# Kernel tuning notes

Measured on AMD Instinct MI355X. Metric: run time of the kernel, lower is better.

## Reference

```python
import jax, jax.numpy as jnp
import numpy as np

# model dims
B, L, C, P, D, NB = 8, 512, 862, 96, 128, 2   # batch, seq_len, enc_in, pred_len, d_model, e_layers
I = 2 * D                                     # mLSTM inner (up-projection factor 2)
NH = 4                                        # mLSTM heads
DH = I // NH                                  # head dim
KDEC = 25                                     # series-decomp moving-average kernel
CK = 4                                        # causal conv kernel in mLSTM layer
EPS = 1e-5


def _ln(x, g):
    m = jnp.mean(x, -1, keepdims=True)
    v = jnp.var(x, -1, keepdims=True)
    return (x - m) * jax.lax.rsqrt(v + EPS) * g


def _mlstm_block(x, p):
    """Pre-LN residual mLSTM block (parallel stabilized formulation)."""
    (lng, Wup, bup, Wc, bc, Wq, Wk, Wv, Wi, bi, Wf, bf, mhg, skip, Wdn, bdn) = p
    Bn, S, _ = x.shape
    y = _ln(x, lng)
    up = y @ Wup + bup                       # [B,S,2I]
    x_in, z = jnp.split(up, 2, axis=-1)      # [B,S,I] each
    # causal depthwise conv (kernel CK) + SiLU
    xc = jax.lax.conv_general_dilated(
        x_in, Wc, window_strides=(1,), padding=((CK - 1, 0),),
        dimension_numbers=('NWC', 'WIO', 'NWC'), feature_group_count=I) + bc
    xc = jax.nn.silu(xc)
    q = xc @ Wq
    k = xc @ Wk
    v = x_in @ Wv
    g_in = jnp.concatenate([q, k, v], -1)    # [B,S,3I]
    ig = (g_in @ Wi + bi).transpose(0, 2, 1)  # [B,NH,S] input-gate preact
    fg = (g_in @ Wf + bf).transpose(0, 2, 1)  # [B,NH,S] forget-gate preact
    qh = q.reshape(Bn, S, NH, DH).transpose(0, 2, 1, 3)
    kh = k.reshape(Bn, S, NH, DH).transpose(0, 2, 1, 3) * (DH ** -0.5)
    vh = v.reshape(Bn, S, NH, DH).transpose(0, 2, 1, 3)
    logf = jax.nn.log_sigmoid(fg)            # [B,NH,S]
    cum = jnp.cumsum(logf, -1)               # inclusive cumsum
    # logD[t,s] = sum_{u=s+1..t} logf_u + i_s  (s<=t)
    logD = cum[..., :, None] - cum[..., None, :] + ig[..., None, :]
    mask = jnp.tril(jnp.ones((S, S), bool))
    logD = jnp.where(mask, logD, -jnp.inf)
    m = jnp.max(logD, -1, keepdims=True)     # row-wise stabilizer [B,NH,S,1]
    Dm = jnp.exp(logD - m)
    scores = jnp.einsum('bhtd,bhsd->bhts', qh, kh) * Dm
    norm = jnp.maximum(jnp.abs(jnp.sum(scores, -1, keepdims=True)), jnp.exp(-m))
    h = jnp.einsum('bhts,bhsd->bhtd', scores / norm, vh)  # [B,NH,S,DH]
    h = h.transpose(0, 2, 1, 3)              # [B,S,NH,DH]
    # multi-head layernorm (per-head, weight only)
    mu = jnp.mean(h, -1, keepdims=True)
    va = jnp.var(h, -1, keepdims=True)
    hn = ((h - mu) * jax.lax.rsqrt(va + EPS)).reshape(Bn, S, I) * mhg
    hs = (hn + skip * xc) * jax.nn.silu(z)
    return x + hs @ Wdn + bdn


def setup_inputs() -> dict:
    key = jax.random.key(0)
    ks = iter(jax.random.split(key, 32))
    f32 = jnp.float32
    def n(shape, s=0.02):
        return jax.random.normal(next(ks), shape, dtype=f32) * s
    inp = {
        'x_enc': jax.random.normal(next(ks), (B, L, C), f32),
        'x_mark_enc': jax.random.normal(next(ks), (B, L, 4), f32),
        'x_dec': jax.random.normal(next(ks), (B, P, C), f32),
        'x_mark_dec': jax.random.normal(next(ks), (B, P, 4), f32),
        # DLinear-style heads (init 1/seq_len as in the source)
        'Ws': jnp.full((P, L), 1.0 / L, dtype=f32), 'bs': jnp.zeros((P,), f32),
        'Wt': jnp.full((P, L), 1.0 / L, dtype=f32), 'bt': jnp.zeros((P,), f32),
        'Wp1': n((D, P)), 'bp1': jnp.zeros((D,), f32),
        'Wp2': n((P, D)), 'bp2': jnp.zeros((P,), f32),
        # stacked per-block mLSTM params
        'ln_g': jnp.ones((NB, D), f32),
        'Wup': n((NB, D, 2 * I)), 'bup': jnp.zeros((NB, 2 * I), f32),
        'Wconv': n((NB, CK, 1, I), 0.1), 'bconv': jnp.zeros((NB, I), f32),
        'Wq': n((NB, I, I)), 'Wk': n((NB, I, I)), 'Wv': n((NB, I, I)),
        'Wi': n((NB, 3 * I, NH)), 'bi': jnp.zeros((NB, NH), f32),
        'Wf': n((NB, 3 * I, NH)), 'bf': jnp.full((NB, NH), 3.0, dtype=f32),
        'mh_g': jnp.ones((NB, I), f32), 'skip': jnp.ones((NB, I), f32),
        'Wdn': n((NB, I, D)), 'bdn': jnp.zeros((NB, D), f32),
        'post_g': jnp.ones((D,), f32),
    }
    return inp


def reference(x_enc, x_mark_enc, x_dec, x_mark_dec, Ws, bs, Wt, bt, Wp1, bp1,
              Wp2, bp2, ln_g, Wup, bup, Wconv, bconv, Wq, Wk, Wv, Wi, bi, Wf,
              bf, mh_g, skip, Wdn, bdn, post_g):
    # series decomposition: edge-replicated moving average (kernel 25, stride 1)
    pad = (KDEC - 1) // 2
    front = jnp.repeat(x_enc[:, :1, :], pad, axis=1)
    end = jnp.repeat(x_enc[:, -1:, :], pad, axis=1)
    xp = jnp.concatenate([front, x_enc, end], axis=1)          # [B,L+24,C]
    cs = jnp.concatenate([jnp.zeros_like(xp[:, :1]), jnp.cumsum(xp, 1)], 1)
    mm = (cs[:, KDEC:, :] - cs[:, :-KDEC, :]) / KDEC           # [B,L,C]
    res = x_enc - mm
    si = res.transpose(0, 2, 1)                                # [B,C,L]
    ti = mm.transpose(0, 2, 1)
    x = (si @ Ws.T + bs) + (ti @ Wt.T + bt)                    # [B,C,P]
    x = x @ Wp1.T + bp1                                        # [B,C,D]
    for b in range(NB):
        x = _mlstm_block(x, (ln_g[b], Wup[b], bup[b], Wconv[b], bconv[b],
                             Wq[b], Wk[b], Wv[b], Wi[b], bi[b], Wf[b], bf[b],
                             mh_g[b], skip[b], Wdn[b], bdn[b]))
    x = _ln(x, post_g)
    x = x @ Wp2.T + bp2                                        # [B,C,P]
    return x.transpose(0, 2, 1)                                # [B,P,C]
```

## Files before the change

### kernel.cpp

```cpp
#include <hip/hip_runtime.h>
#include <math.h>

#define BB 8
#define LL 512
#define CC 862
#define PP 96
#define DD 128
#define II 256
#define NHH 4
#define DHH 64
#define SS 862
#define BC (BB*CC)
#define VTS 864
#define NITEMS2 896

typedef unsigned short u16;
using bf16x8 = __attribute__((ext_vector_type(8))) short;
using f32x4  = __attribute__((ext_vector_type(4))) float;

__device__ __forceinline__ u16 f2b(float x) {
  union { float f; unsigned u; } v; v.f = x;
  unsigned r = v.u + 0x7FFF + ((v.u >> 16) & 1);
  return (u16)(r >> 16);
}
__device__ __forceinline__ float b2f(u16 h) {
  union { unsigned u; float f; } v; v.u = ((unsigned)h) << 16;
  return v.f;
}

#define XCH(r, c) ((((c) ^ ((r) & 7)) << 3))

__global__ __launch_bounds__(256) void prep_kernel(
    const float* __restrict__ Wup, const float* __restrict__ Wq,
    const float* __restrict__ Wk, const float* __restrict__ Wv,
    const float* __restrict__ Wdn, const float* __restrict__ Ws,
    const float* __restrict__ Wt, const float* __restrict__ Wp1,
    const float* __restrict__ bs, const float* __restrict__ bt,
    const float* __restrict__ bp1, const float* __restrict__ Wi,
    const float* __restrict__ Wf,
    u16* __restrict__ WupT, u16* __restrict__ WqkT,
    u16* __restrict__ WvT, u16* __restrict__ WdnT,
    u16* __restrict__ BTh, float* __restrict__ hbias,
    float* __restrict__ Gc, float* __restrict__ Gv)
{
  int gb = blockIdx.x;
  int tid = threadIdx.x;
  if (gb < 640) {
    int bx = gb & 63, by = gb >> 6;
    const float* src; u16* dst; int R, Cn; float scl = 1.f;
    switch (by) {
      case 0: src = Wup;          dst = WupT;            R = 128; Cn = 512; break;
      case 1: src = Wup + 65536;  dst = WupT + 65536;    R = 128; Cn = 512; break;
      case 2: src = Wq;           dst = WqkT;            R = 256; Cn = 256; scl = 0.125f; break;
      case 3: src = Wk;           dst = WqkT + 65536;    R = 256; Cn = 256; break;
      case 4: src = Wq + 65536;   dst = WqkT + 131072;   R = 256; Cn = 256; scl = 0.125f; break;
      case 5: src = Wk + 65536;   dst = WqkT + 196608;   R = 256; Cn = 256; break;
      case 6: src = Wv;           dst = WvT;             R = 256; Cn = 256; break;
      case 7: src = Wv + 65536;   dst = WvT + 65536;     R = 256; Cn = 256; break;
      case 8: src = Wdn;          dst = WdnT;            R = 256; Cn = 128; break;
      default: src = Wdn + 32768; dst = WdnT + 32768;    R = 256; Cn = 128; break;
    }
    int tpr = Cn >> 5;
    int tx = bx % tpr, ty_ = bx / tpr;
    if (ty_ >= (R >> 5)) return;
    __shared__ float t[32][33];
    int r0 = ty_ * 32, c0 = tx * 32;
    int cr = tid >> 5, cc = tid & 31;
    #pragma unroll
    for (int rr = 0; rr < 4; ++rr)
      t[cr + rr * 8][cc] = src[(size_t)(r0 + cr + rr * 8) * Cn + c0 + cc];
    __syncthreads();
    #pragma unroll
    for (int rr = 0; rr < 4; ++rr)
      dst[(size_t)(c0 + cr + rr * 8) * R + r0 + cc] = f2b(t[cc][cr + rr * 8] * scl);
  } else if (gb < 1152) {
    int i2 = gb - 640;
    int d = i2 & 127, byy = i2 >> 7;
    int lp = byy * 256 + tid;
    const float* wp = Wp1 + d * 96;
    float acc = 0.f;
    if (lp < 512) {
      for (int p = 0; p < 96; ++p) acc += Ws[p * 512 + lp] * wp[p];
    } else {
      int l = lp - 512;
      for (int p = 0; p < 96; ++p) acc += (Wt[p * 512 + l] - Ws[p * 512 + l]) * wp[p];
    }
    BTh[(size_t)d * 1024 + lp] = f2b(acc);
  } else if (gb == 1152) {
    if (tid < 128) {
      float acc = bp1[tid];
      for (int p = 0; p < 96; ++p) acc += (bs[p] + bt[p]) * Wp1[tid * 96 + p];
      hbias[tid] = acc;
    }
  } else {
    int i2 = gb - 1153;
    int i = i2 & 255, blk = i2 >> 8;
    int j = tid;
    float wq = Wq[(size_t)blk * 65536 + i * 256 + j];
    float wk = Wk[(size_t)blk * 65536 + i * 256 + j];
    float wv = Wv[(size_t)blk * 65536 + i * 256 + j];
    const float* wi = Wi + blk * 3072;
    const float* wf = Wf + blk * 3072;
    float pc[8], pv[8];
    #pragma unroll
    for (int o = 0; o < 4; ++o) {
      pc[o]     = wq * wi[j * 4 + o] + wk * wi[(256 + j) * 4 + o];
      pc[4 + o] = wq * wf[j * 4 + o] + wk * wf[(256 + j) * 4 + o];
      pv[o]     = wv * wi[(512 + j) * 4 + o];
      pv[4 + o] = wv * wf[(512 + j) * 4 + o];
    }
    #pragma unroll
    for (int o = 0; o < 8; ++o)
      #pragma unroll
      for (int d = 1; d < 64; d <<= 1) {
        pc[o] += __shfl_xor(pc[o], d);
        pv[o] += __shfl_xor(pv[o], d);
      }
    __shared__ float red[4][16];
    int wv_ = j >> 6, lane = j & 63;
    if (lane == 0) {
      #pragma unroll
      for (int o = 0; o < 8; ++o) { red[wv_][o] = pc[o]; red[wv_][8 + o] = pv[o]; }
    }
    __syncthreads();
    if (j < 16) {
      float s4 = red[0][j] + red[1][j] + red[2][j] + red[3][j];
      if (j < 8) Gc[((size_t)blk * 256 + i) * 8 + j] = s4;
      else       Gv[((size_t)blk * 256 + i) * 8 + j - 8] = s4;
    }
  }
}

__global__ __launch_bounds__(256) void ta_kernel(
    const float* __restrict__ xe, u16* __restrict__ Ah)
{
  __shared__ float xel[16][545];
  __shared__ float mml[16][517];
  int tid = threadIdx.x;
  int b = blockIdx.x / 54, ct = blockIdx.x % 54;
  int c0 = ct * 16;
  for (int j = 0; j < 34; ++j) {
    int idx = tid + j * 256;
    if (idx < 8576) {
      int li = idx >> 4, cc = idx & 15;
      int l = li - 12; l = l < 0 ? 0 : (l > 511 ? 511 : l);
      int c = c0 + cc; if (c > 861) c = 861;
      xel[cc][li] = xe[((size_t)b * LL + l) * CC + c];
    }
  }
  __syncthreads();
  {
    int cl = tid & 15;
    int l0 = (tid >> 4) * 32;
    float win = 0.f;
    #pragma unroll 5
    for (int o = 0; o < 25; ++o) win += xel[cl][l0 + o];
    mml[cl][l0] = win * (1.f / 25.f);
    for (int i = 1; i < 32; ++i) {
      win += xel[cl][l0 + 24 + i] - xel[cl][l0 + i - 1];
      mml[cl][l0 + i] = win * (1.f / 25.f);
    }
  }
  __syncthreads();
  for (int j = 0; j < 32; ++j) {
    int idx = tid + j * 256;
    int cr = idx >> 9, l = idx & 511;
    int c = c0 + cr;
    if (c < CC) {
      size_t base = ((size_t)b * CC + c) * 1024;
      Ah[base + l] = f2b(xel[cr][12 + l]);
      Ah[base + 512 + l] = f2b(mml[cr][l]);
    }
  }
}

__device__ __forceinline__ void gemm_core(
    const u16* __restrict__ A, int lda, const u16* __restrict__ BT, int ldbt,
    int M, int K, int m0, int n0, int tid,
    u16 (*As0)[40], u16 (*As1)[40], u16 (*Bs0)[40], u16 (*Bs1)[40],
    f32x4 acc[2][2])
{
  int wv = tid >> 6, lane = tid & 63;
  int wr = wv >> 1, wc = wv & 1;
  int lrow = lane & 15, lk = lane >> 4;
  int arow = tid >> 2, aseg = tid & 3;
  for (int k0 = 0; k0 < K; k0 += 64) {
    int gm = m0 + arow; if (gm > M - 1) gm = M - 1;
    const u16* ap = &A[(size_t)gm * lda + k0 + aseg * 8];
    *(uint4*)&As0[arow][aseg * 8] = *(const uint4*)ap;
    *(uint4*)&As1[arow][aseg * 8] = *(const uint4*)(ap + 32);
    const u16* bp = &BT[(size_t)(n0 + arow) * ldbt + k0 + aseg * 8];
    *(uint4*)&Bs0[arow][aseg * 8] = *(const uint4*)bp;
    *(uint4*)&Bs1[arow][aseg * 8] = *(const uint4*)(bp + 32);
    __syncthreads();
    bf16x8 af[2], bfr[2];
    #pragma unroll
    for (int fm = 0; fm < 2; ++fm) af[fm] = *(const bf16x8*)&As0[wr * 32 + fm * 16 + lrow][lk * 8];
    #pragma unroll
    for (int fn = 0; fn < 2; ++fn) bfr[fn] = *(const bf16x8*)&Bs0[wc * 32 + fn * 16 + lrow][lk * 8];
    #pragma unroll
    for (int fm = 0; fm < 2; ++fm)
      #pragma unroll
      for (int fn = 0; fn < 2; ++fn)
        acc[fm][fn] = __builtin_amdgcn_mfma_f32_16x16x32_bf16(af[fm], bfr[fn], acc[fm][fn], 0, 0, 0);
    #pragma unroll
    for (int fm = 0; fm < 2; ++fm) af[fm] = *(const bf16x8*)&As1[wr * 32 + fm * 16 + lrow][lk * 8];
    #pragma unroll
    for (int fn = 0; fn < 2; ++fn) bfr[fn] = *(const bf16x8*)&Bs1[wc * 32 + fn * 16 + lrow][lk * 8];
    #pragma unroll
    for (int fm = 0; fm < 2; ++fm)
      #pragma unroll
      for (int fn = 0; fn < 2; ++fn)
        acc[fm][fn] = __builtin_amdgcn_mfma_f32_16x16x32_bf16(af[fm], bfr[fn], acc[fm][fn], 0, 0, 0);
    __syncthreads();
  }
}

template<int MODE>
__global__ __launch_bounds__(256) void gemm_bf16(
    const u16* __restrict__ A, int lda,
    const u16* __restrict__ BT, int ldbt,
    float* __restrict__ C, int ldc, const float* __restrict__ bias,
    int M, int N, int K)
{
  __shared__ u16 As0[64][40], As1[64][40];
  __shared__ u16 Bs0[64][40], Bs1[64][40];
  int tid = threadIdx.x;
  int m0 = blockIdx.y * 64, n0 = blockIdx.x * 64;
  f32x4 acc[2][2] = {};
  gemm_core(A, lda, BT, ldbt, M, K, m0, n0, tid, As0, As1, Bs0, Bs1, acc);
  int wv = tid >> 6, lane = tid & 63;
  int wr = wv >> 1, wc = wv & 1;
  int lrow = lane & 15, lk = lane >> 4;
  #pragma unroll
  for (int fm = 0; fm < 2; ++fm) {
    #pragma unroll
    for (int fn = 0; fn < 2; ++fn) {
      int col = n0 + wc * 32 + fn * 16 + lrow;
      #pragma unroll
      for (int r = 0; r < 4; ++r) {
        int row = m0 + wr * 32 + fm * 16 + lk * 4 + r;
        if (row < M) {
          float vv = acc[fm][fn][r];
          if (bias) vv += bias[col];
          float* cp = &C[(size_t)row * ldc + col];
          if (MODE == 1) vv += *cp;
          *cp = vv;
        }
      }
    }
  }
}

template<int MODE, int OUTF32>
__global__ __launch_bounds__(256) void gemm_ln(
    const u16* __restrict__ A, int lda,
    const u16* __restrict__ BT, int ldbt,
    float* __restrict__ x, const float* __restrict__ bias,
    const float* __restrict__ g,
    float* __restrict__ y, u16* __restrict__ y_bf,
    int M, int K)
{
  __shared__ u16 As0[32][40], As1[32][40];
  __shared__ u16 Bs0[128][40], Bs1[128][40];
  __shared__ float red_s[32][2], red_q[32][2];
  int tid = threadIdx.x;
  int m0 = blockIdx.x * 32;
  int wv = tid >> 6, lane = tid & 63;
  int wr = wv >> 1, wc = wv & 1;
  int lrow = lane & 15, lk = lane >> 4;
  f32x4 acc[4] = {};
  int arow = tid >> 3, aseg7 = tid & 7;
  int brow = tid >> 1, bhalf = tid & 1;
  for (int k0 = 0; k0 < K; k0 += 64) {
    int gm = m0 + arow; if (gm > M - 1) gm = M - 1;
    const u16* ap = &A[(size_t)gm * lda + k0];
    if (aseg7 < 4) *(uint4*)&As0[arow][aseg7 * 8] = *(const uint4*)(ap + aseg7 * 8);
    else           *(uint4*)&As1[arow][(aseg7 - 4) * 8] = *(const uint4*)(ap + 32 + (aseg7 - 4) * 8);
    const u16* bp = &BT[(size_t)brow * ldbt + k0];
    #pragma unroll
    for (int j = 0; j < 2; ++j) {
      int seg = bhalf * 2 + j;
      *(uint4*)&Bs0[brow][seg * 8] = *(const uint4*)(bp + seg * 8);
      *(uint4*)&Bs1[brow][seg * 8] = *(const uint4*)(bp + 32 + seg * 8);
    }
    __syncthreads();
    bf16x8 af, bfr[4];
    af = *(const bf16x8*)&As0[wr * 16 + lrow][lk * 8];
    #pragma unroll
    for (int fn = 0; fn < 4; ++fn) bfr[fn] = *(const bf16x8*)&Bs0[wc * 64 + fn * 16 + lrow][lk * 8];
    #pragma unroll
    for (int fn = 0; fn < 4; ++fn)
      acc[fn] = __builtin_amdgcn_mfma_f32_16x16x32_bf16(af, bfr[fn], acc[fn], 0, 0, 0);
    af = *(const bf16x8*)&As1[wr * 16 + lrow][lk * 8];
    #pragma unroll
    for (int fn = 0; fn < 4; ++fn) bfr[fn] = *(const bf16x8*)&Bs1[wc * 64 + fn * 16 + lrow][lk * 8];
    #pragma unroll
    for (int fn = 0; fn < 4; ++fn)
      acc[fn] = __builtin_amdgcn_mfma_f32_16x16x32_bf16(af, bfr[fn], acc[fn], 0, 0, 0);
    __syncthreads();
  }
  #pragma unroll
  for (int r = 0; r < 4; ++r) {
    int lrid = wr * 16 + lk * 4 + r;
    int grow = m0 + lrid;
    float sr = 0.f, sq = 0.f;
    #pragma unroll
    for (int fn = 0; fn < 4; ++fn) {
      int col = wc * 64 + fn * 16 + lrow;
      float vv = acc[fn][r] + bias[col];
      if (MODE == 1) vv += x[(size_t)grow * DD + col];
      acc[fn][r] = vv;
      if (grow < M) x[(size_t)grow * DD + col] = vv;
      sr += vv; sq += vv * vv;
    }
    sr += __shfl_xor(sr, 1); sq += __shfl_xor(sq, 1);
    sr += __shfl_xor(sr, 2); sq += __shfl_xor(sq, 2);
    sr += __shfl_xor(sr, 4); sq += __shfl_xor(sq, 4);
    sr += __shfl_xor(sr, 8); sq += __shfl_xor(sq, 8);
    if (lrow == 0) { red_s[lrid][wc] = sr; red_q[lrid][wc] = sq; }
  }
  __syncthreads();
  #pragma unroll
  for (int r = 0; r < 4; ++r) {
    int lrid = wr * 16 + lk * 4 + r;
    int grow = m0 + lrid;
    if (grow >= M) continue;
    float s = red_s[lrid][0] + red_s[lrid][1];
    float q = red_q[lrid][0] + red_q[lrid][1];
    float mean = s * (1.f / 128.f);
    float var = q * (1.f / 128.f) - mean * mean;
    float rr = rsqrtf(var + 1e-5f);
    #pragma unroll
    for (int fn = 0; fn < 4; ++fn) {
      int col = wc * 64 + fn * 16 + lrow;
      float out = (acc[fn][r] - mean) * rr * g[col];
      if (OUTF32) y[(size_t)grow * DD + col] = out;
      else        y_bf[(size_t)grow * DD + col] = f2b(out);
    }
  }
}

__global__ __launch_bounds__(256) void qkv_kernel(
    const u16* __restrict__ xc_bf, const u16* __restrict__ xin_bf,
    const u16* __restrict__ WqkT, const u16* __restrict__ WvT,
    u16* __restrict__ qkh, u16* __restrict__ qkl,
    u16* __restrict__ vhT, u16* __restrict__ vlT)
{
  __shared__ u16 As0[64][40], As1[64][40];
  __shared__ u16 Bs0[64][40], Bs1[64][40];
  int tid = threadIdx.x;
  int m0 = blockIdx.y * 64;
  bool is_qk = blockIdx.x < 8;
  int n0 = (is_qk ? blockIdx.x : blockIdx.x - 8) * 64;
  const u16* A  = is_qk ? xc_bf : xin_bf;
  const u16* BT = is_qk ? WqkT : WvT;
  f32x4 acc[2][2] = {};
  gemm_core(A, 256, BT, 256, BC, 256, m0, n0, tid, As0, As1, Bs0, Bs1, acc);
  int wv = tid >> 6, lane = tid & 63;
  int wr = wv >> 1, wc = wv & 1;
  int lrow = lane & 15, lk = lane >> 4;
  #pragma unroll
  for (int fm = 0; fm < 2; ++fm) {
    #pragma unroll
    for (int fn = 0; fn < 2; ++fn) {
      int col = n0 + wc * 32 + fn * 16 + lrow;
      int rbase = m0 + wr * 32 + fm * 16 + lk * 4;
      if (is_qk) {
        #pragma unroll
        for (int r = 0; r < 4; ++r) {
          int row = rbase + r;
          if (row < BC) {
            float vv = acc[fm][fn][r];
            u16 hi = f2b(vv);
            u16 lo = f2b(vv - b2f(hi));
            qkh[(size_t)row * 512 + col] = hi;
            qkl[(size_t)row * 512 + col] = lo;
          }
        }
      } else {
        u16 hi4[4], lo4[4];
        #pragma unroll
        for (int r = 0; r < 4; ++r) {
          float vv = acc[fm][fn][r];
          hi4[r] = f2b(vv);
          lo4[r] = f2b(vv - b2f(hi4[r]));
        }
        int bb0 = rbase / SS, s0_ = rbase - bb0 * SS;
        int bb3 = (rbase + 3) / SS;
        if (bb0 == bb3 && rbase + 3 < BC) {
          size_t o = ((size_t)bb0 * II + col) * VTS + s0_;
          *(unsigned*)&vhT[o]     = (unsigned)hi4[0] | ((unsigned)hi4[1] << 16);
          *(unsigned*)&vhT[o + 2] = (unsigned)hi4[2] | ((unsigned)hi4[3] << 16);
          *(unsigned*)&vlT[o]     = (unsigned)lo4[0] | ((unsigned)lo4[1] << 16);
          *(unsigned*)&vlT[o + 2] = (unsigned)lo4[2] | ((unsigned)lo4[3] << 16);
        } else {
          #pragma unroll
          for (int r = 0; r < 4; ++r) {
            int row = rbase + r;
            if (row < BC) {
              int bb = row / SS, s = row - bb * SS;
              size_t o = ((size_t)bb * II + col) * VTS + s;
              vhT[o] = hi4[r];
              vlT[o] = lo4[r];
            }
          }
        }
      }
    }
  }
}

__global__ __launch_bounds__(256) void conv_gates_kernel(
    const float* __restrict__ up, const float* __restrict__ Wc,
    const float* __restrict__ bc, const float* __restrict__ Gc,
    const float* __restrict__ Gv, const float* __restrict__ bi,
    const float* __restrict__ bfp,
    float* __restrict__ xc, u16* __restrict__ xc_bf, u16* __restrict__ xin_bf,
    float* __restrict__ ig, float* __restrict__ fg)
{
  __shared__ float red[4][8];
  int row = blockIdx.x;
  int i = threadIdx.x;
  int b = row / SS, s = row - b * SS;
  float acc = bc[i];
  float xin = 0.f;
  #pragma unroll
  for (int w2 = 0; w2 < 4; ++w2) {
    int sp = s - 3 + w2;
    if (sp >= 0) {
      float uv = up[((size_t)b * SS + sp) * 512 + i];
      acc += uv * Wc[w2 * 256 + i];
      if (w2 == 3) xin = uv;
    }
  }
  float sg = 1.f / (1.f + __expf(-acc));
  float val = acc * sg;
  xc[(size_t)row * II + i] = val;
  xc_bf[(size_t)row * II + i] = f2b(val);
  xin_bf[(size_t)row * II + i] = f2b(xin);
  float p[8];
  const float* gci = &Gc[i * 8];
  const float* gvi = &Gv[i * 8];
  #pragma unroll
  for (int o = 0; o < 8; ++o) p[o] = val * gci[o] + xin * gvi[o];
  #pragma unroll
  for (int o = 0; o < 8; ++o)
    #pragma unroll
    for (int d = 1; d < 64; d <<= 1) p[o] += __shfl_xor(p[o], d);
  int wv = i >> 6, lane = i & 63;
  if (lane == 0) {
    #pragma unroll
    for (int o = 0; o < 8; ++o) red[wv][o] = p[o];
  }
  __syncthreads();
  if (i < 8) {
    float sum = red[0][i] + red[1][i] + red[2][i] + red[3][i];
    if (i < 4) ig[((size_t)b * NHH + i) * SS + s] = sum + bi[i];
    else       fg[((size_t)b * NHH + i - 4) * SS + s] = sum + bfp[i - 4];
  }
}

__device__ __forceinline__ float logsig(float x) {
  return fminf(x, 0.f) - log1pf(__expf(-fabsf(x)));
}

__global__ __launch_bounds__(64) void scan_kernel(
    const float* __restrict__ fg, const float* __restrict__ ig,
    float* __restrict__ cumf, float* __restrict__ aa, float* __restrict__ MMb)
{
  int bh = blockIdx.x;
  int lane = threadIdx.x;
  const float* f = fg + (size_t)bh * SS;
  const float* g = ig + (size_t)bh * SS;
  int s0 = lane * 14, s1 = s0 + 14; if (s1 > SS) s1 = SS;
  float loc = 0.f;
  for (int s = s0; s < s1; ++s) loc += logsig(f[s]);
  float v = loc;
  #pragma unroll
  for (int d = 1; d < 64; d <<= 1) { float o = __shfl_up(v, d); if (lane >= d) v += o; }
  float run = v - loc;
  float lmax = -1e30f;
  for (int s = s0; s < s1; ++s) {
    run += logsig(f[s]);
    cumf[(size_t)bh * SS + s] = run;
    float a = g[s] - run;
    aa[(size_t)bh * SS + s] = a;
    lmax = fmaxf(lmax, a);
  }
  float mv = lmax;
  #pragma unroll
  for (int d = 1; d < 64; d <<= 1) { float o = __shfl_up(mv, d); if (lane >= d) mv = fmaxf(mv, o); }
  float em = __shfl_up(mv, 1);
  if (lane == 0) em = -1e30f;
  float runm = em;
  for (int s = s0; s < s1; ++s) {
    runm = fmaxf(runm, aa[(size_t)bh * SS + s]);
    MMb[(size_t)bh * SS + s] = runm;
  }
}

__global__ __launch_bounds__(256) void attn_kernel(
    const u16* __restrict__ qkh, const u16* __restrict__ qkl,
    const u16* __restrict__ vhT, const u16* __restrict__ vlT,
    const float* __restrict__ aab, const float* __restrict__ MMb,
    float* __restrict__ pacc, float* __restrict__ pw)
{
  __shared__ u16 KWh[64][64], KWl[64][64];
  __shared__ u16 Vh[64][64], Vl[64][64];
  __shared__ float a_lds[64];
  int tid = threadIdx.x;
  int wv = tid >> 6, lane = tid & 63;
  int lr = lane & 15, lg = lane >> 4;
  int item = blockIdx.x;
  int pp = item >> 5;
  int tb = 13 - (pp >> 1);
  int part = pp & 1;
  int h = item & 3, b = (item >> 2) & 7;
  int t0 = tb * 64;
  int nt = tb + 1;
  int nt0 = (nt + 1) >> 1;
  int st_begin = part ? nt0 : 0;
  int st_end   = part ? nt : nt0;
  const float* aabh = aab + ((size_t)b * NHH + h) * SS;
  const float* Mbh  = MMb + ((size_t)b * NHH + h) * SS;

  int tq = t0 + wv * 16 + lr; if (tq > SS - 1) tq = SS - 1;
  const u16* qrow_h = qkh + ((size_t)b * SS + tq) * 512 + h * 64;
  const u16* qrow_l = qkl + ((size_t)b * SS + tq) * 512 + h * 64;
  bf16x8 qh0 = *(const bf16x8*)(qrow_h + lg * 8);
  bf16x8 qh1 = *(const bf16x8*)(qrow_h + 32 + lg * 8);
  bf16x8 ql0 = *(const bf16x8*)(qrow_l + lg * 8);
  bf16x8 ql1 = *(const bf16x8*)(qrow_l + 32 + lg * 8);

  float Mt[4];
  #pragma unroll
  for (int r = 0; r < 4; ++r) {
    int t = t0 + wv * 16 + lg * 4 + r; int tc = t < SS ? t : SS - 1;
    Mt[r] = Mbh[tc];
  }

  int row = tid >> 2, seg = tid & 3;
  const u16* vrow_h = vhT + ((size_t)(b * II + h * 64 + row)) * VTS + seg * 16;
  const u16* vrow_l = vlT + ((size_t)(b * II + h * 64 + row)) * VTS + seg * 16;

  f32x4 hacc[4] = {};
  float wsum[4] = {0.f, 0.f, 0.f, 0.f};

  uint4 rk0, rk1, rk2, rk3, rv0, rv1, rv2, rv3;
  float ra = -1e30f;
  if (st_begin < st_end) {
    int sg = st_begin * 64 + row;
    int sc = sg < SS ? sg : SS - 1;
    const u16* kp  = qkh + ((size_t)b * SS + sc) * 512 + 256 + h * 64 + seg * 16;
    const u16* klp = qkl + ((size_t)b * SS + sc) * 512 + 256 + h * 64 + seg * 16;
    rk0 = *(const uint4*)kp;  rk1 = *(const uint4*)(kp + 8);
    rk2 = *(const uint4*)klp; rk3 = *(const uint4*)(klp + 8);
    int sn = st_begin * 64;
    rv0 = *(const uint4*)(vrow_h + sn); rv1 = *(const uint4*)(vrow_h + sn + 8);
    rv2 = *(const uint4*)(vrow_l + sn); rv3 = *(const uint4*)(vrow_l + sn + 8);
    if (tid < 64) ra = (sn + tid < SS) ? aabh[sn + tid] : -1e30f;
  }

  for (int st = st_begin; st < st_end; ++st) {
    int s0 = st * 64;
    __syncthreads();
    *(uint4*)&KWh[row][XCH(row, 2 * seg)]     = rk0;
    *(uint4*)&KWh[row][XCH(row, 2 * seg + 1)] = rk1;
    *(uint4*)&KWl[row][XCH(row, 2 * seg)]     = rk2;
    *(uint4*)&KWl[row][XCH(row, 2 * seg + 1)] = rk3;
    *(uint4*)&Vh[row][XCH(row, 2 * seg)]     = rv0;
    *(uint4*)&Vh[row][XCH(row, 2 * seg + 1)] = rv1;
    *(uint4*)&Vl[row][XCH(row, 2 * seg)]     = rv2;
    *(uint4*)&Vl[row][XCH(row, 2 * seg + 1)] = rv3;
    if (tid < 64) a_lds[tid] = ra;
    if (st + 1 < st_end) {
      int sn = s0 + 64;
      int sg = sn + row;
      int sc = sg < SS ? sg : SS - 1;
      const u16* kp  = qkh + ((size_t)b * SS + sc) * 512 + 256 + h * 64 + seg * 16;
      const u16* klp = qkl + ((size_t)b * SS + sc) * 512 + 256 + h * 64 + seg * 16;
      rk0 = *(const uint4*)kp;  rk1 = *(const uint4*)(kp + 8);
      rk2 = *(const uint4*)klp; rk3 = *(const uint4*)(klp + 8);
      rv0 = *(const uint4*)(vrow_h + sn); rv1 = *(const uint4*)(vrow_h + sn + 8);
      rv2 = *(const uint4*)(vrow_l + sn); rv3 = *(const uint4*)(vrow_l + sn + 8);
      if (tid < 64) ra = (sn + tid < SS) ? aabh[sn + tid] : -1e30f;
    }
    __syncthreads();
    float am = a_lds[lane];
    #pragma unroll
    for (int dd = 1; dd < 64; dd <<= 1) am = fmaxf(am, __shfl_xor(am, dd));
    f32x4 p[4];
    #pragma unroll
    for (int sf = 0; sf < 4; ++sf) {
      int sr = sf * 16 + lr;
      bf16x8 kh0 = *(const bf16x8*)&KWh[sr][XCH(sr, lg)];
      bf16x8 kh1 = *(const bf16x8*)&KWh[sr][XCH(sr, lg + 4)];
      bf16x8 kl0 = *(const bf16x8*)&KWl[sr][XCH(sr, lg)];
      bf16x8 kl1 = *(const bf16x8*)&KWl[sr][XCH(sr, lg + 4)];
      f32x4 acc = {};
      acc = __builtin_amdgcn_mfma_f32_16x16x32_bf16(qh0, kl0, acc, 0, 0, 0);
      acc = __builtin_amdgcn_mfma_f32_16x16x32_bf16(qh1, kl1, acc, 0, 0, 0);
      acc = __builtin_amdgcn_mfma_f32_16x16x32_bf16(ql0, kh0, acc, 0, 0, 0);
      acc = __builtin_amdgcn_mfma_f32_16x16x32_bf16(ql1, kh1, acc, 0, 0, 0);
      acc = __builtin_amdgcn_mfma_f32_16x16x32_bf16(qh0, kh0, acc, 0, 0, 0);
      acc = __builtin_amdgcn_mfma_f32_16x16x32_bf16(qh1, kh1, acc, 0, 0, 0);
      p[sf] = acc;
    }
    __syncthreads();
    float ee[4], ft[4];
    #pragma unroll
    for (int sf = 0; sf < 4; ++sf) ee[sf] = __expf(a_lds[sf * 16 + lr] - am);
    #pragma unroll
    for (int r = 0; r < 4; ++r) ft[r] = __expf(fminf(am - Mt[r], 80.f));
    #pragma unroll
    for (int sf = 0; sf < 4; ++sf) {
      int s = s0 + sf * 16 + lr;
      int sc_ = sf * 2 + (lr >> 3), sb = lr & 7;
      #pragma unroll
      for (int r = 0; r < 4; ++r) {
        int tl_ = wv * 16 + lg * 4 + r;
        int t = t0 + tl_;
        float wval = (s <= t) ? p[sf][r] * ee[sf] * ft[r] : 0.f;
        wsum[r] += wval;
        u16 hi_ = f2b(wval);
        u16 lo_ = f2b(wval - b2f(hi_));
        KWh[tl_][XCH(tl_, sc_) + sb] = hi_;
        KWl[tl_][XCH(tl_, sc_) + sb] = lo_;
      }
    }
    __syncthreads();
    int tr = wv * 16 + lr;
    bf16x8 wh0 = *(const bf16x8*)&KWh[tr][XCH(tr, lg)];
    bf16x8 wh1 = *(const bf16x8*)&KWh[tr][XCH(tr, lg + 4)];
    bf16x8 wl0 = *(const bf16x8*)&KWl[tr][XCH(tr, lg)];
    bf16x8 wl1 = *(const bf16x8*)&KWl[tr][XCH(tr, lg + 4)];
    #pragma unroll
    for (int df = 0; df < 4; ++df) {
      int dr = df * 16 + lr;
      bf16x8 vh0 = *(const bf16x8*)&Vh[dr][XCH(dr, lg)];
      bf16x8 vh1 = *(const bf16x8*)&Vh[dr][XCH(dr, lg + 4)];
      bf16x8 vl0 = *(const bf16x8*)&Vl[dr][XCH(dr, lg)];
      bf16x8 vl1 = *(const bf16x8*)&Vl[dr][XCH(dr, lg + 4)];
      f32x4 a2 = hacc[df];
      a2 = __builtin_amdgcn_mfma_f32_16x16x32_bf16(wh0, vl0, a2, 0, 0, 0);
      a2 = __builtin_amdgcn_mfma_f32_16x16x32_bf16(wh1, vl1, a2, 0, 0, 0);
      a2 = __builtin_amdgcn_mfma_f32_16x16x32_bf16(wl0, vh0, a2, 0, 0, 0);
      a2 = __builtin_amdgcn_mfma_f32_16x16x32_bf16(wl1, vh1, a2, 0, 0, 0);
      a2 = __builtin_amdgcn_mfma_f32_16x16x32_bf16(wh0, vh0, a2, 0, 0, 0);
      a2 = __builtin_amdgcn_mfma_f32_16x16x32_bf16(wh1, vh1, a2, 0, 0, 0);
      hacc[df] = a2;
    }
  }
  #pragma unroll
  for (int r = 0; r < 4; ++r) {
    float sgn = wsum[r];
    sgn += __shfl_xor(sgn, 1); sgn += __shfl_xor(sgn, 2);
    sgn += __shfl_xor(sgn, 4); sgn += __shfl_xor(sgn, 8);
    wsum[r] = sgn;
  }
  float* pa = pacc + (size_t)part * BC * II;
  #pragma unroll
  for (int r = 0; r < 4; ++r) {
    int t = t0 + wv * 16 + lg * 4 + r;
    if (t < SS) {
      #pragma unroll
      for (int df = 0; df < 4; ++df)
        pa[((size_t)b * SS + t) * II + h * 64 + df * 16 + lr] = hacc[df][r];
      if (lr == 0)
        pw[(((size_t)part * BB + b) * NHH + h) * SS + t] = wsum[r];
    }
  }
}

__global__ __launch_bounds__(256) void combine_mhln_kernel(
    const float* __restrict__ pacc, const float* __restrict__ pw,
    const float* __restrict__ cumf, const float* __restrict__ MMb,
    const float* __restrict__ up, const float* __restrict__ xc,
    const float* __restrict__ mhg, const float* __restrict__ skip,
    u16* __restrict__ hb_bf)
{
  int row = blockIdx.x;
  int i = threadIdx.x;
  int h = i >> 6, lane = i & 63;
  int b = row / SS, s = row - b * SS;
  size_t bhS = ((size_t)b * NHH + h) * SS + s;
  float v = pacc[(size_t)row * II + i] + pacc[(size_t)BC * II + (size_t)row * II + i];
  float wsum = pw[bhS] + pw[(size_t)BB * NHH * SS + bhS];
  float nfl = __expf(-(cumf[bhS] + MMb[bhS]));
  float hv = v / fmaxf(fabsf(wsum), nfl);
  float sm = hv, sq = hv * hv;
  #pragma unroll
  for (int d = 1; d < 64; d <<= 1) { sm += __shfl_xor(sm, d); sq += __shfl_xor(sq, d); }
  float mu = sm * (1.f / 64.f);
  float var = sq * (1.f / 64.f) - mu * mu;
  float hn = (hv - mu) * rsqrtf(var + 1e-5f) * mhg[i];
  float z = up[(size_t)row * 512 + 256 + i];
  float sil = z / (1.f + __expf(-z));
  hb_bf[(size_t)row * II + i] = f2b((hn + skip[i] * xc[(size_t)row * II + i]) * sil);
}

__global__ __launch_bounds__(256) void final_kernel(
    const float* __restrict__ y, const float* __restrict__ Wp2,
    const float* __restrict__ bp2, float* __restrict__ out)
{
  __shared__ float yl[32 * 132];
  __shared__ float ol[96 * 32];
  int tid = threadIdx.x;
  int blk = blockIdx.x;
  int b = blk / 27, ct = blk % 27;
  int c0 = ct * 32;
  int nc = CC - c0; if (nc > 32) nc = 32;
  for (int j = 0; j < 16; ++j) {
    int idx = tid + j * 256;
    int cl = idx >> 7, d2 = idx & 127;
    yl[cl * 132 + d2] = (cl < nc) ? y[((size_t)b * CC + c0 + cl) * DD + d2] : 0.f;
  }
  __syncthreads();
  for (int j = 0; j < 12; ++j) {
    int o = tid + j * 256;
    int p = o >> 5, cl = o & 31;
    const float* wr = Wp2 + p * 128;
    float acc = bp2[p];
    #pragma unroll 8
    for (int d0 = 0; d0 < 128; d0 += 4) {
      float4 yv = *(const float4*)&yl[cl * 132 + d0];
      float4 wv = *(const float4*)&wr[d0];
      acc += yv.x * wv.x + yv.y * wv.y + yv.z * wv.z + yv.w * wv.w;
    }
    ol[p * 32 + cl] = acc;
  }
  __syncthreads();
  for (int j = 0; j < 12; ++j) {
    int o = tid + j * 256;
    int p = o >> 5, cl = o & 31;
    if (cl < nc) out[(size_t)b * PP * CC + (size_t)p * CC + c0 + cl] = ol[p * 32 + cl];
  }
}

extern "C" void kernel_launch(void* const* d_in, const int* in_sizes, int n_in,
                              void* d_out, int out_size, void* d_ws, size_t ws_size,
                              hipStream_t stream) {
  const float* xe   = (const float*)d_in[0];
  const float* Ws   = (const float*)d_in[4];
  const float* bs   = (const float*)d_in[5];
  const float* Wt_  = (const float*)d_in[6];
  const float* bt   = (const float*)d_in[7];
  const float* Wp1  = (const float*)d_in[8];
  const float* bp1  = (const float*)d_in[9];
  const float* Wp2  = (const float*)d_in[10];
  const float* bp2  = (const float*)d_in[11];
  const float* lng  = (const float*)d_in[12];
  const float* Wup  = (const float*)d_in[13];
  const float* bup  = (const float*)d_in[14];
  const float* Wcv  = (const float*)d_in[15];
  const float* bcv  = (const float*)d_in[16];
  const float* Wq   = (const float*)d_in[17];
  const float* Wk   = (const float*)d_in[18];
  const float* Wv   = (const float*)d_in[19];
  const float* Wi   = (const float*)d_in[20];
  const float* bi   = (const float*)d_in[21];
  const float* Wf   = (const float*)d_in[22];
  const float* bf_  = (const float*)d_in[23];
  const float* mhg  = (const float*)d_in[24];
  const float* skp  = (const float*)d_in[25];
  const float* Wdn  = (const float*)d_in[26];
  const float* bdn  = (const float*)d_in[27];
  const float* pg   = (const float*)d_in[28];
  float* out = (float*)d_out;

  float* w   = (float*)d_ws;
  float* x   = w;
  float* y   = x   + 882688;
  float* up  = y   + 882688;
  float* xc  = up  + 3530752;
  float* pacc = xc + 1765376;
  float* pw  = pacc + 3530752;
  float* ig  = pw  + 55168;
  float* fg  = ig  + 27584;
  float* cum = fg  + 27584;
  float* aab = cum + 27584;
  float* MMb = aab + 27584;
  float* hbias = MMb + 27584;
  float* Gc  = hbias + 128;
  float* Gv  = Gc + 4096;
  u16* ub    = (u16*)(Gv + 4096);
  u16* y_bf  = ub;            ub += 6896 * 128;
  u16* xc_bf = ub;            ub += 6896 * 256;
  u16* xin_bf = ub;           ub += 6896 * 256;
  u16* hb_bf = ub;            ub += 6896 * 256;
  u16* qkh   = ub;            ub += 6896 * 512;
  u16* qkl   = ub;            ub += 6896 * 512;
  u16* vhT   = ub;            ub += 8 * 256 * VTS;
  u16* vlT   = ub;            ub += 8 * 256 * VTS;
  u16* BTh   = ub;            ub += 131072;
  u16* WupT  = ub;            ub += 131072;
  u16* WqkT  = ub;            ub += 262144;
  u16* WvT   = ub;            ub += 131072;
  u16* WdnT  = ub;            ub += 65536;
  u16* Ah = (u16*)up;

  prep_kernel<<<1665, 256, 0, stream>>>(
      Wup, Wq, Wk, Wv, Wdn, Ws, Wt_, Wp1, bs, bt, bp1, Wi, Wf,
      WupT, WqkT, WvT, WdnT, BTh, hbias, Gc, Gv);

  ta_kernel<<<432, 256, 0, stream>>>(xe, Ah);
  gemm_ln<0, 0><<<216, 256, 0, stream>>>(
      Ah, 1024, BTh, 1024, x, hbias, lng, nullptr, y_bf, BC, 1024);

  for (int blk = 0; blk < 2; ++blk) {
    gemm_bf16<0><<<dim3(8, 108), 256, 0, stream>>>(
        y_bf, 128, WupT + blk * 65536, 128, up, 512, bup + blk * 512, BC, 512, 128);
    conv_gates_kernel<<<6896, 256, 0, stream>>>(
        up, Wcv + blk * 1024, bcv + blk * 256, Gc + blk * 2048, Gv + blk * 2048,
        bi + blk * 4, bf_ + blk * 4, xc, xc_bf, xin_bf, ig, fg);
    qkv_kernel<<<dim3(12, 108), 256, 0, stream>>>(
        xc_bf, xin_bf, WqkT + blk * 131072, WvT + blk * 65536,
        qkh, qkl, vhT, vlT);
    scan_kernel<<<32, 64, 0, stream>>>(fg, ig, cum, aab, MMb);
    attn_kernel<<<NITEMS2, 256, 0, stream>>>(qkh, qkl, vhT, vlT, aab, MMb, pacc, pw);
    combine_mhln_kernel<<<6896, 256, 0, stream>>>(
        pacc, pw, cum, MMb, up, xc, mhg + blk * 256, skp + blk * 256, hb_bf);
    if (blk == 0)
      gemm_ln<1, 0><<<216, 256, 0, stream>>>(
          hb_bf, 256, WdnT, 256, x, bdn, lng + 128, nullptr, y_bf, BC, 256);
    else
      gemm_ln<1, 1><<<216, 256, 0, stream>>>(
          hb_bf, 256, WdnT + 32768, 256, x, bdn + 128, pg, y, nullptr, BC, 256);
  }

  final_kernel<<<216, 256, 0, stream>>>(y, Wp2, bp2, out);
}
```

Baseline: 276.7 us.

## Fuse mLSTM combine/headnorm into down-proj GEMM A-load and merge scan into qkv

Removes the combine_mhln kernel: the down-projection GEMM+LN now computes the normalized, gated mLSTM output directly while loading its A tile, so the intermediate bf16 hb buffer is no longer written and re-read. The scan kernel is also folded into the qkv GEMM launch as 32 extra blocks, which cuts launches and lets the scan overlap the GEMM. The catch is that the fused A-load does more scalar fp32 loads and transcendental work inside the GEMM's K loop, with only 216 blocks to hide that latency.

```diff
diff --git a/kernel.cpp b/kernel.cpp
--- a/kernel.cpp
+++ b/kernel.cpp
@@ -252,14 +252,18 @@
   }
 }
 
-template<int MODE, int OUTF32>
+template<int MODE, int OUTF32, int FUSEC>
 __global__ __launch_bounds__(256) void gemm_ln(
     const u16* __restrict__ A, int lda,
     const u16* __restrict__ BT, int ldbt,
     float* __restrict__ x, const float* __restrict__ bias,
     const float* __restrict__ g,
     float* __restrict__ y, u16* __restrict__ y_bf,
-    int M, int K)
+    int M, int K,
+    const float* __restrict__ pacc, const float* __restrict__ pw,
+    const float* __restrict__ cumf, const float* __restrict__ MMb,
+    const float* __restrict__ up2, const float* __restrict__ xc2,
+    const float* __restrict__ mhg, const float* __restrict__ skip)
 {
   __shared__ u16 As0[32][40], As1[32][40];
   __shared__ u16 Bs0[128][40], Bs1[128][40];
@@ -274,9 +278,44 @@
   int brow = tid >> 1, bhalf = tid & 1;
   for (int k0 = 0; k0 < K; k0 += 64) {
     int gm = m0 + arow; if (gm > M - 1) gm = M - 1;
-    const u16* ap = &A[(size_t)gm * lda + k0];
-    if (aseg7 < 4) *(uint4*)&As0[arow][aseg7 * 8] = *(const uint4*)(ap + aseg7 * 8);
-    else           *(uint4*)&As1[arow][(aseg7 - 4) * 8] = *(const uint4*)(ap + 32 + (aseg7 - 4) * 8);
+    if (FUSEC == 0) {
+      const u16* ap = &A[(size_t)gm * lda + k0];
+      if (aseg7 < 4) *(uint4*)&As0[arow][aseg7 * 8] = *(const uint4*)(ap + aseg7 * 8);
+      else           *(uint4*)&As1[arow][(aseg7 - 4) * 8] = *(const uint4*)(ap + 32 + (aseg7 - 4) * 8);
+    } else {
+      int bb = gm / SS, sx = gm - bb * SS;
+      int hh = k0 >> 6;
+      size_t bhS = ((size_t)bb * NHH + hh) * SS + sx;
+      float wsum = pw[bhS] + pw[(size_t)BB * NHH * SS + bhS];
+      float nfl = __expf(-(cumf[bhS] + MMb[bhS]));
+      float rden = 1.f / fmaxf(fabsf(wsum), nfl);
+      int colb = k0 + aseg7 * 8;
+      const float* p0 = &pacc[(size_t)gm * II + colb];
+      const float* p1 = p0 + (size_t)BC * II;
+      float hv[8], sr = 0.f, sq2 = 0.f;
+      #pragma unroll
+      for (int j = 0; j < 8; ++j) {
+        hv[j] = (p0[j] + p1[j]) * rden;
+        sr += hv[j]; sq2 += hv[j] * hv[j];
+      }
+      sr += __shfl_xor(sr, 1); sq2 += __shfl_xor(sq2, 1);
+      sr += __shfl_xor(sr, 2); sq2 += __shfl_xor(sq2, 2);
+      sr += __shfl_xor(sr, 4); sq2 += __shfl_xor(sq2, 4);
+      float mu = sr * (1.f / 64.f);
+      float var = sq2 * (1.f / 64.f) - mu * mu;
+      float rr2 = rsqrtf(var + 1e-5f);
+      u16 o8[8];
+      #pragma unroll
+      for (int j = 0; j < 8; ++j) {
+        int col = colb + j;
+        float hn = (hv[j] - mu) * rr2 * mhg[col];
+        float z = up2[(size_t)gm * 512 + 256 + col];
+        float sil = z / (1.f + __expf(-z));
+        o8[j] = f2b((hn + skip[col] * xc2[(size_t)gm * II + col]) * sil);
+      }
+      if (aseg7 < 4) *(uint4*)&As0[arow][aseg7 * 8] = *(const uint4*)o8;
+      else           *(uint4*)&As1[arow][(aseg7 - 4) * 8] = *(const uint4*)o8;
+    }
     const u16* bp = &BT[(size_t)brow * ldbt + k0];
     #pragma unroll
     for (int j = 0; j < 2; ++j) {
@@ -341,18 +380,59 @@
   }
 }
 
-__global__ __launch_bounds__(256) void qkv_kernel(
+__device__ __forceinline__ float logsig(float x) {
+  return fminf(x, 0.f) - log1pf(__expf(-fabsf(x)));
+}
+
+__global__ __launch_bounds__(256) void qkv_scan_kernel(
     const u16* __restrict__ xc_bf, const u16* __restrict__ xin_bf,
     const u16* __restrict__ WqkT, const u16* __restrict__ WvT,
     u16* __restrict__ qkh, u16* __restrict__ qkl,
-    u16* __restrict__ vhT, u16* __restrict__ vlT)
+    u16* __restrict__ vhT, u16* __restrict__ vlT,
+    const float* __restrict__ fg, const float* __restrict__ ig,
+    float* __restrict__ cumf, float* __restrict__ aa, float* __restrict__ MMb)
 {
   __shared__ u16 As0[64][40], As1[64][40];
   __shared__ u16 Bs0[64][40], Bs1[64][40];
   int tid = threadIdx.x;
-  int m0 = blockIdx.y * 64;
-  bool is_qk = blockIdx.x < 8;
-  int n0 = (is_qk ? blockIdx.x : blockIdx.x - 8) * 64;
+  int bx = blockIdx.x;
+  if (bx >= 1296) {
+    if (tid >= 64) return;
+    int bh = bx - 1296;
+    int lane = tid;
+    const float* f = fg + (size_t)bh * SS;
+    const float* gg = ig + (size_t)bh * SS;
+    int s0 = lane * 14, s1 = s0 + 14; if (s1 > SS) s1 = SS;
+    float loc = 0.f;
+    for (int s = s0; s < s1; ++s) loc += logsig(f[s]);
+    float v = loc;
+    #pragma unroll
+    for (int d = 1; d < 64; d <<= 1) { float o = __shfl_up(v, d); if (lane >= d) v += o; }
+    float run = v - loc;
+    float lmax = -1e30f;
+    for (int s = s0; s < s1; ++s) {
+      run += logsig(f[s]);
+      cumf[(size_t)bh * SS + s] = run;
+      float a = gg[s] - run;
+      aa[(size_t)bh * SS + s] = a;
+      lmax = fmaxf(lmax, a);
+    }
+    float mv = lmax;
+    #pragma unroll
+    for (int d = 1; d < 64; d <<= 1) { float o = __shfl_up(mv, d); if (lane >= d) mv = fmaxf(mv, o); }
+    float em = __shfl_up(mv, 1);
+    if (lane == 0) em = -1e30f;
+    float runm = em;
+    for (int s = s0; s < s1; ++s) {
+      runm = fmaxf(runm, aa[(size_t)bh * SS + s]);
+      MMb[(size_t)bh * SS + s] = runm;
+    }
+    return;
+  }
+  int m0 = (bx / 12) * 64;
+  int nrole = bx % 12;
+  bool is_qk = nrole < 8;
+  int n0 = (is_qk ? nrole : nrole - 8) * 64;
   const u16* A  = is_qk ? xc_bf : xin_bf;
   const u16* BT = is_qk ? WqkT : WvT;
   f32x4 acc[2][2] = {};
@@ -461,45 +541,6 @@
   }
 }
 
-__device__ __forceinline__ float logsig(float x) {
-  return fminf(x, 0.f) - log1pf(__expf(-fabsf(x)));
-}
-
-__global__ __launch_bounds__(64) void scan_kernel(
-    const float* __restrict__ fg, const float* __restrict__ ig,
-    float* __restrict__ cumf, float* __restrict__ aa, float* __restrict__ MMb)
-{
-  int bh = blockIdx.x;
-  int lane = threadIdx.x;
-  const float* f = fg + (size_t)bh * SS;
-  const float* g = ig + (size_t)bh * SS;
-  int s0 = lane * 14, s1 = s0 + 14; if (s1 > SS) s1 = SS;
-  float loc = 0.f;
-  for (int s = s0; s < s1; ++s) loc += logsig(f[s]);
-  float v = loc;
-  #pragma unroll
-  for (int d = 1; d < 64; d <<= 1) { float o = __shfl_up(v, d); if (lane >= d) v += o; }
-  float run = v - loc;
-  float lmax = -1e30f;
-  for (int s = s0; s < s1; ++s) {
-    run += logsig(f[s]);
-    cumf[(size_t)bh * SS + s] = run;
-    float a = g[s] - run;
-    aa[(size_t)bh * SS + s] = a;
-    lmax = fmaxf(lmax, a);
-  }
-  float mv = lmax;
-  #pragma unroll
-  for (int d = 1; d < 64; d <<= 1) { float o = __shfl_up(mv, d); if (lane >= d) mv = fmaxf(mv, o); }
-  float em = __shfl_up(mv, 1);
-  if (lane == 0) em = -1e30f;
-  float runm = em;
-  for (int s = s0; s < s1; ++s) {
-    runm = fmaxf(runm, aa[(size_t)bh * SS + s]);
-    MMb[(size_t)bh * SS + s] = runm;
-  }
-}
-
 __global__ __launch_bounds__(256) void attn_kernel(
     const u16* __restrict__ qkh, const u16* __restrict__ qkl,
     const u16* __restrict__ vhT, const u16* __restrict__ vlT,
@@ -671,33 +712,6 @@
         pw[(((size_t)part * BB + b) * NHH + h) * SS + t] = wsum[r];
     }
   }
-}
-
-__global__ __launch_bounds__(256) void combine_mhln_kernel(
-    const float* __restrict__ pacc, const float* __restrict__ pw,
-    const float* __restrict__ cumf, const float* __restrict__ MMb,
-    const float* __restrict__ up, const float* __restrict__ xc,
-    const float* __restrict__ mhg, const float* __restrict__ skip,
-    u16* __restrict__ hb_bf)
-{
-  int row = blockIdx.x;
-  int i = threadIdx.x;
-  int h = i >> 6, lane = i & 63;
-  int b = row / SS, s = row - b * SS;
-  size_t bhS = ((size_t)b * NHH + h) * SS + s;
-  float v = pacc[(size_t)row * II + i] + pacc[(size_t)BC * II + (size_t)row * II + i];
-  float wsum = pw[bhS] + pw[(size_t)BB * NHH * SS + bhS];
-  float nfl = __expf(-(cumf[bhS] + MMb[bhS]));
-  float hv = v / fmaxf(fabsf(wsum), nfl);
-  float sm = hv, sq = hv * hv;
-  #pragma unroll
-  for (int d = 1; d < 64; d <<= 1) { sm += __shfl_xor(sm, d); sq += __shfl_xor(sq, d); }
-  float mu = sm * (1.f / 64.f);
-  float var = sq * (1.f / 64.f) - mu * mu;
-  float hn = (hv - mu) * rsqrtf(var + 1e-5f) * mhg[i];
-  float z = up[(size_t)row * 512 + 256 + i];
-  float sil = z / (1.f + __expf(-z));
-  hb_bf[(size_t)row * II + i] = f2b((hn + skip[i] * xc[(size_t)row * II + i]) * sil);
 }
 
 __global__ __launch_bounds__(256) void final_kernel(
@@ -788,7 +802,6 @@
   u16* y_bf  = ub;            ub += 6896 * 128;
   u16* xc_bf = ub;            ub += 6896 * 256;
   u16* xin_bf = ub;           ub += 6896 * 256;
-  u16* hb_bf = ub;            ub += 6896 * 256;
   u16* qkh   = ub;            ub += 6896 * 512;
   u16* qkl   = ub;            ub += 6896 * 512;
   u16* vhT   = ub;            ub += 8 * 256 * VTS;
@@ -805,8 +818,9 @@
       WupT, WqkT, WvT, WdnT, BTh, hbias, Gc, Gv);
 
   ta_kernel<<<432, 256, 0, stream>>>(xe, Ah);
-  gemm_ln<0, 0><<<216, 256, 0, stream>>>(
-      Ah, 1024, BTh, 1024, x, hbias, lng, nullptr, y_bf, BC, 1024);
+  gemm_ln<0, 0, 0><<<216, 256, 0, stream>>>(
+      Ah, 1024, BTh, 1024, x, hbias, lng, nullptr, y_bf, BC, 1024,
+      nullptr, nullptr, nullptr, nullptr, nullptr, nullptr, nullptr, nullptr);
 
   for (int blk = 0; blk < 2; ++blk) {
     gemm_bf16<0><<<dim3(8, 108), 256, 0, stream>>>(
@@ -814,19 +828,18 @@
     conv_gates_kernel<<<6896, 256, 0, stream>>>(
         up, Wcv + blk * 1024, bcv + blk * 256, Gc + blk * 2048, Gv + blk * 2048,
         bi + blk * 4, bf_ + blk * 4, xc, xc_bf, xin_bf, ig, fg);
-    qkv_kernel<<<dim3(12, 108), 256, 0, stream>>>(
+    qkv_scan_kernel<<<1328, 256, 0, stream>>>(
         xc_bf, xin_bf, WqkT + blk * 131072, WvT + blk * 65536,
-        qkh, qkl, vhT, vlT);
-    scan_kernel<<<32, 64, 0, stream>>>(fg, ig, cum, aab, MMb);
+        qkh, qkl, vhT, vlT, fg, ig, cum, aab, MMb);
     attn_kernel<<<NITEMS2, 256, 0, stream>>>(qkh, qkl, vhT, vlT, aab, MMb, pacc, pw);
-    combine_mhln_kernel<<<6896, 256, 0, stream>>>(
-        pacc, pw, cum, MMb, up, xc, mhg + blk * 256, skp + blk * 256, hb_bf);
     if (blk == 0)
-      gemm_ln<1, 0><<<216, 256, 0, stream>>>(
-          hb_bf, 256, WdnT, 256, x, bdn, lng + 128, nullptr, y_bf, BC, 256);
+      gemm_ln<1, 0, 1><<<216, 256, 0, stream>>>(
+          nullptr, 0, WdnT, 256, x, bdn, lng + 128, nullptr, y_bf, BC, 256,
+          pacc, pw, cum, MMb, up, xc, mhg, skp);
     else
-      gemm_ln<1, 1><<<216, 256, 0, stream>>>(
-          hb_bf, 256, WdnT + 32768, 256, x, bdn + 128, pg, y, nullptr, BC, 256);
+      gemm_ln<1, 1, 1><<<216, 256, 0, stream>>>(
+          nullptr, 0, WdnT + 32768, 256, x, bdn + 128, pg, y, nullptr, BC, 256,
+          pacc, pw, cum, MMb, up, xc, mhg + 256, skp + 256);
   }
 
   final_kernel<<<216, 256, 0, stream>>>(y, Wp2, bp2, out);
```

Result: faster. 255.3 us (-7.7%).
